# Kernel tuning notes

Measured on AMD Instinct MI355X. Metric: run time of the kernel, lower is better.

The kernel has to match this reference:

```python
import jax, jax.numpy as jnp
import numpy as np

B, C, H, W = 16, 1024, 32, 32  # H*W must equal C (required by matmul(h, fg) in the source)
EPS = 1e-5
NEG_SLOPE = 0.01


def setup_inputs() -> dict:
    key = jax.random.key(0)
    ks = jax.random.split(key, 12)
    s = 1.0 / np.sqrt(C)
    inp = {"x": jax.random.normal(ks[0], (B, C, H, W), jnp.float32)}
    for i, name in enumerate(["f", "g", "h", "c"]):
        inp[f"W{name}"] = jax.random.normal(ks[1 + 2 * i], (C, C), jnp.float32) * s
        inp[f"b{name}"] = jax.random.normal(ks[2 + 2 * i], (C,), jnp.float32) * 0.01
    inp["gamma"] = jnp.ones((C,), jnp.float32)
    inp["beta"] = jnp.zeros((C,), jnp.float32)
    inp["rmean"] = jax.random.normal(ks[9], (C,), jnp.float32) * 0.01
    inp["rvar"] = jax.random.uniform(ks[10], (C,), jnp.float32, 0.5, 1.5)
    return inp


def reference(x, Wf, bf, Wg, bg, Wh, bh, Wc, bc, gamma, beta, rmean, rvar):
    b, c, h_, w_ = x.shape
    n = h_ * w_  # == c by construction
    xf = x.reshape(b, c, n)

    def proj(Wp, bp):  # 1x1 conv == per-pixel channel matmul
        return jnp.einsum('oc,bcn->bon', Wp, xf) + bp[None, :, None]

    f = proj(Wf, bf)              # (B, C, N)
    g = proj(Wg, bg)              # (B, C, N); transposed(1,2) handled in einsum
    hh = proj(Wh, bh)             # (B, C, N)
    scores = jnp.einsum('bcn,bdn->bcd', f, g)        # f @ g^T -> (B, C, C)
    attn = jax.nn.softmax(scores, axis=1)            # softmax over dim=1 (as in source)
    # dropout2d(p=0.5) is identity in eval mode
    hfg = jnp.einsum('bcn,bnd->bcd', hh, attn)       # matmul(h, fg), needs N == C
    hfg = hfg.reshape(b, c, h_, w_)
    y = jnp.einsum('oc,bchw->bohw', Wc, hfg) + bc[None, :, None, None]
    y = jnp.where(y >= 0, y, NEG_SLOPE * y)          # LeakyReLU
    inv = gamma / jnp.sqrt(rvar + EPS)               # BatchNorm (eval mode)
    y = (y - rmean[None, :, None, None]) * inv[None, :, None, None] + beta[None, :, None, None]
    return y + x
```

## Files before the change

kernel.cpp:

```cpp
#include <hip/hip_runtime.h>
#include <cstdint>
#include <cstddef>

using half8  = __attribute__((ext_vector_type(8))) _Float16;
using half4  = __attribute__((ext_vector_type(4))) _Float16;
using float4v = __attribute__((ext_vector_type(4))) float;

#define CD 1024
#define M2 (1024 * 1024)

#define GLD16(gp, lp)                                                          \
    __builtin_amdgcn_global_load_lds(                                          \
        (const __attribute__((address_space(1))) void*)(gp),                   \
        (__attribute__((address_space(3))) void*)(lp), 16, 0, 0)

__global__ void prep_weights(const float* __restrict__ Wf, const float* __restrict__ Wg,
                             const float* __restrict__ Wh, const float* __restrict__ Wc,
                             const float* __restrict__ bf, const float* __restrict__ bg,
                             const float* __restrict__ bh,
                             _Float16* __restrict__ Wfgh, _Float16* __restrict__ WcH,
                             float* __restrict__ bstack) {
    int idx = blockIdx.x * 256 + threadIdx.x;
    if (idx < 3 * M2) {
        const float* s = idx < M2 ? Wf : (idx < 2 * M2 ? Wg : Wh);
        int off = idx & (M2 - 1);
        Wfgh[idx] = (_Float16)s[off];
    } else if (idx < 4 * M2) {
        WcH[idx - 3 * M2] = (_Float16)Wc[idx - 3 * M2];
    } else if (idx < 4 * M2 + 3 * CD) {
        int j = idx - 4 * M2;
        const float* s = j < CD ? bf : (j < 2 * CD ? bg : bh);
        bstack[j] = s[j & (CD - 1)];
    }
}

__global__ void transpose_x(const float* __restrict__ x, _Float16* __restrict__ xT, int b0) {
    __shared__ float tile[32][33];
    int z = blockIdx.z;
    const float* xb = x + (size_t)(b0 + z) * M2;
    _Float16* xTb = xT + (size_t)z * M2;
    int n0 = blockIdx.x * 32, k0 = blockIdx.y * 32;
    int tx = threadIdx.x, ty = threadIdx.y;
#pragma unroll
    for (int i = 0; i < 4; i++)
        tile[ty + i * 8][tx] = xb[(size_t)(k0 + ty + i * 8) * CD + n0 + tx];
    __syncthreads();
#pragma unroll
    for (int i = 0; i < 4; i++)
        xTb[(size_t)(n0 + ty + i * 8) * CD + k0 + tx] = (_Float16)tile[tx][ty + i * 8];
}

__global__ __launch_bounds__(256) void gemv_bch(const float* __restrict__ Wc,
                                                const float* __restrict__ bh,
                                                float* __restrict__ bch) {
    int o = blockIdx.x * 4 + (threadIdx.x >> 6);
    int lane = threadIdx.x & 63;
    float s = 0.f;
    for (int c = lane; c < CD; c += 64) s += Wc[(size_t)o * CD + c] * bh[c];
#pragma unroll
    for (int off = 32; off > 0; off >>= 1) s += __shfl_xor(s, off);
    if (lane == 0) bch[o] = s;
}

__global__ __launch_bounds__(256) void gemm128(const _Float16* __restrict__ A,
                                               const _Float16* __restrict__ B,
                                               _Float16* __restrict__ C) {
    __shared__ __align__(16) _Float16 As[128][32];
    __shared__ __align__(16) _Float16 Bs[128][32];
    int row0 = blockIdx.y * 128, col0 = blockIdx.x * 128;
    int tid = threadIdx.x, lane = tid & 63, wave = tid >> 6;
    int wr = wave >> 1, wc = wave & 1;
    const int srow = lane >> 2;
    const int scol = (lane & 3) * 8;
    const size_t gA0 = (size_t)(row0 + wave * 16 + srow) * 1024 + scol;
    const size_t gA1 = gA0 + (size_t)64 * 1024;
    const size_t gB0 = (size_t)(col0 + wave * 16 + srow) * 1024 + scol;
    const size_t gB1 = gB0 + (size_t)64 * 1024;
    _Float16* ldsA0 = &As[wave * 16][0];
    _Float16* ldsA1 = &As[64 + wave * 16][0];
    _Float16* ldsB0 = &Bs[wave * 16][0];
    _Float16* ldsB1 = &Bs[64 + wave * 16][0];
    float4v acc[4][4] = {};
    const int kq = (lane >> 4) * 8, rl = lane & 15;
    for (int kt = 0; kt < 1024; kt += 32) {
        GLD16(A + gA0 + kt, ldsA0);
        GLD16(A + gA1 + kt, ldsA1);
        GLD16(B + gB0 + kt, ldsB0);
        GLD16(B + gB1 + kt, ldsB1);
        __syncthreads();
        half8 af[4], bfr[4];
#pragma unroll
        for (int m = 0; m < 4; m++) af[m] = *(const half8*)(&As[wr * 64 + m * 16 + rl][kq]);
#pragma unroll
        for (int n = 0; n < 4; n++) bfr[n] = *(const half8*)(&Bs[wc * 64 + n * 16 + rl][kq]);
#pragma unroll
        for (int m = 0; m < 4; m++)
#pragma unroll
            for (int n = 0; n < 4; n++)
                acc[m][n] = __builtin_amdgcn_mfma_f32_16x16x32_f16(af[m], bfr[n], acc[m][n], 0, 0, 0);
        __syncthreads();
    }
#pragma unroll
    for (int m = 0; m < 4; m++)
#pragma unroll
        for (int r = 0; r < 4; r++) {
            int row = row0 + wr * 64 + m * 16 + ((lane >> 4) << 2) + r;
#pragma unroll
            for (int n = 0; n < 4; n++) {
                int col = col0 + wc * 64 + n * 16 + (lane & 15);
                C[(size_t)row * 1024 + col] = (_Float16)acc[m][n][r];
            }
        }
}

__global__ __launch_bounds__(256) void softmax_col(const float* __restrict__ ST,
                                                   _Float16* __restrict__ attnT) {
    int d = blockIdx.x, z = blockIdx.y;
    const float* row = ST + ((size_t)z * CD + d) * CD;
    _Float16* orow = attnT + ((size_t)z * CD + d) * CD;
    int t = threadIdx.x;
    float4v v = *(const float4v*)(row + t * 4);
    float mx = fmaxf(fmaxf(v[0], v[1]), fmaxf(v[2], v[3]));
#pragma unroll
    for (int o = 32; o > 0; o >>= 1) mx = fmaxf(mx, __shfl_xor(mx, o));
    __shared__ float redm[4], reds[4];
    int wave = t >> 6, lane = t & 63;
    if (lane == 0) redm[wave] = mx;
    __syncthreads();
    mx = fmaxf(fmaxf(redm[0], redm[1]), fmaxf(redm[2], redm[3]));
    float e[4];
    float s = 0.f;
#pragma unroll
    for (int i = 0; i < 4; i++) {
        e[i] = __expf(v[i] - mx);
        s += e[i];
    }
#pragma unroll
    for (int o = 32; o > 0; o >>= 1) s += __shfl_xor(s, o);
    if (lane == 0) reds[wave] = s;
    __syncthreads();
    s = reds[0] + reds[1] + reds[2] + reds[3];
    float inv = 1.0f / s;
    half4 ov;
#pragma unroll
    for (int i = 0; i < 4; i++) ov[i] = (_Float16)(e[i] * inv);
    *(half4*)(orow + t * 4) = ov;
}

enum { EP_F16B = 0, EP_F32 = 1, EP_F16 = 2, EP_FIN = 3 };

#define STG_A(T, BUF)                                                          \
    GLD16(gA + (size_t)(T) * 64 + 0 * 8192, &As[BUF][wv * 32 + 0][0]);         \
    GLD16(gA + (size_t)(T) * 64 + 1 * 8192, &As[BUF][wv * 32 + 8][0]);         \
    GLD16(gA + (size_t)(T) * 64 + 2 * 8192, &As[BUF][wv * 32 + 16][0]);        \
    GLD16(gA + (size_t)(T) * 64 + 3 * 8192, &As[BUF][wv * 32 + 24][0]);
#define STG_B(T, BUF)                                                          \
    GLD16(gB + (size_t)(T) * 64 + 0 * 8192, &Bs[BUF][wv * 32 + 0][0]);         \
    GLD16(gB + (size_t)(T) * 64 + 1 * 8192, &Bs[BUF][wv * 32 + 8][0]);         \
    GLD16(gB + (size_t)(T) * 64 + 2 * 8192, &Bs[BUF][wv * 32 + 16][0]);        \
    GLD16(gB + (size_t)(T) * 64 + 3 * 8192, &Bs[BUF][wv * 32 + 24][0]);

#define READS(SET, BUF, COL)                                                   \
    _Pragma("unroll") for (int m = 0; m < 8; m++)                              \
        a##SET[m] = *(const half8*)&As[BUF][wr * 128 + m * 16 + rl][COL];      \
    _Pragma("unroll") for (int n = 0; n < 4; n++)                              \
        b##SET[n] = *(const half8*)&Bs[BUF][wc * 64 + n * 16 + rl][COL];

#define MFMA32(SET)                                                            \
    __builtin_amdgcn_s_setprio(1);                                             \
    _Pragma("unroll") for (int m = 0; m < 8; m++)                              \
        _Pragma("unroll") for (int n = 0; n < 4; n++)                          \
            acc[m][n] = __builtin_amdgcn_mfma_f32_16x16x32_f16(                \
                a##SET[m], b##SET[n], acc[m][n], 0, 0, 0);                     \
    __builtin_amdgcn_s_setprio(0);

#define TILE64(BUF, OBUF, DOSTAGE, STT)                                        \
    {                                                                          \
        asm volatile("s_waitcnt vmcnt(0)" ::: "memory");                       \
        __builtin_amdgcn_sched_barrier(0);                                     \
        __builtin_amdgcn_s_barrier();                                          \
        READS(0, BUF, c0)                                                      \
        if (DOSTAGE) { STG_A(STT, OBUF) }                                      \
        MFMA32(0)                                                              \
        READS(1, BUF, c1)                                                      \
        if (DOSTAGE) { STG_B(STT, OBUF) }                                      \
        MFMA32(1)                                                              \
    }

template <int EPI>
__global__ __launch_bounds__(512, 2) void gemm_nt(
    const _Float16* __restrict__ A, int64_t sA, const _Float16* __restrict__ B, int64_t sB,
    void* __restrict__ Cp, int64_t sC, const float* __restrict__ bias,
    const float* __restrict__ bc, const float* __restrict__ gamma,
    const float* __restrict__ beta, const float* __restrict__ rmean,
    const float* __restrict__ rvar, const float* __restrict__ xres) {
    __shared__ __align__(16) _Float16 As[2][256][64];
    __shared__ __align__(16) _Float16 Bs[2][256][64];
    int z = blockIdx.z;
    const _Float16* Ab = A + (size_t)z * sA;
    const _Float16* Bb = B + (size_t)z * sB;
    int row0 = blockIdx.y * 256, col0 = blockIdx.x * 256;
    int tid = threadIdx.x, lane = tid & 63, wv = tid >> 6;
    int wr = wv >> 2, wc = wv & 3;

    const _Float16* gA = Ab + (size_t)(row0 + wv * 32 + (lane >> 3)) * 1024 +
                         ((lane & 7) ^ (lane >> 3)) * 8;
    const _Float16* gB = Bb + (size_t)(col0 + wv * 32 + (lane >> 3)) * 1024 +
                         ((lane & 7) ^ (lane >> 3)) * 8;

    const int rl = lane & 15;
    const int q = lane >> 4;
    const int c0 = ((q) ^ (rl & 7)) * 8;
    const int c1 = ((q + 4) ^ (rl & 7)) * 8;

    float4v acc[8][4] = {};
    half8 a0[8], b0[4], a1[8], b1[4];

    STG_A(0, 0) STG_B(0, 0)

#pragma unroll 1
    for (int g = 0; g < 7; ++g) {
        int t = 2 * g;
        TILE64(0, 1, 1, t + 1)
        TILE64(1, 0, 1, t + 2)
    }
    TILE64(0, 1, 1, 15)
    TILE64(1, 0, 0, 0)

#pragma unroll
    for (int m = 0; m < 8; m++) {
#pragma unroll
        for (int r = 0; r < 4; r++) {
            int row = row0 + wr * 128 + m * 16 + ((lane >> 4) << 2) + r;
            float add0 = 0.f, mu = 0.f, invs = 1.f, bet = 0.f;
            if constexpr (EPI == EP_F16B) add0 = bias[row];
            if constexpr (EPI == EP_FIN) {
                add0 = bc[row];
                mu = rmean[row];
                invs = gamma[row] * rsqrtf(rvar[row] + 1e-5f);
                bet = beta[row];
            }
#pragma unroll
            for (int n = 0; n < 4; n++) {
                int col = col0 + wc * 64 + n * 16 + (lane & 15);
                float v = acc[m][n][r];
                if constexpr (EPI == EP_F16B) {
                    ((_Float16*)Cp)[(size_t)z * sC + (size_t)row * 1024 + col] = (_Float16)(v + add0);
                } else if constexpr (EPI == EP_F32) {
                    ((float*)Cp)[(size_t)z * sC + (size_t)row * 1024 + col] = v;
                } else if constexpr (EPI == EP_F16) {
                    ((_Float16*)Cp)[(size_t)z * sC + (size_t)row * 1024 + col] = (_Float16)v;
                } else {
                    v += add0;
                    v = v >= 0.f ? v : 0.01f * v;
                    v = (v - mu) * invs + bet;
                    v += xres[(size_t)z * M2 + (size_t)row * 1024 + col];
                    ((float*)Cp)[(size_t)z * sC + (size_t)row * 1024 + col] = v;
                }
            }
        }
    }
}

extern "C" void kernel_launch(void* const* d_in, const int* in_sizes, int n_in,
                              void* d_out, int out_size, void* d_ws, size_t ws_size,
                              hipStream_t stream) {
    const float* x = (const float*)d_in[0];
    const float* Wf = (const float*)d_in[1];
    const float* bf = (const float*)d_in[2];
    const float* Wg = (const float*)d_in[3];
    const float* bg = (const float*)d_in[4];
    const float* Wh = (const float*)d_in[5];
    const float* bh = (const float*)d_in[6];
    const float* Wc = (const float*)d_in[7];
    const float* bc = (const float*)d_in[8];
    const float* gamma = (const float*)d_in[9];
    const float* beta = (const float*)d_in[10];
    const float* rmean = (const float*)d_in[11];
    const float* rvar = (const float*)d_in[12];

    char* p = (char*)d_ws;
    _Float16* Wfgh = (_Float16*)p;
    p += (size_t)3 * M2 * 2;
    _Float16* WcH = (_Float16*)p;
    p += (size_t)M2 * 2;
    float* bstack = (float*)p;
    p += (size_t)3 * CD * 4;
    size_t fixed = (size_t)(p - (char*)d_ws);
    fixed = (fixed + 255) & ~(size_t)255;

    size_t perB = (size_t)2 * M2 + (size_t)6 * M2 + (size_t)4 * M2;
    int nb = 16;
    while (nb > 1 && fixed + (size_t)nb * perB > ws_size) nb >>= 1;

    char* q = (char*)d_ws + fixed;

    {
        int total = 4 * M2 + 3 * CD;
        prep_weights<<<dim3((total + 255) / 256), dim3(256), 0, stream>>>(
            Wf, Wg, Wh, Wc, bf, bg, bh, Wfgh, WcH, bstack);
    }
    {
        _Float16* WhT = (_Float16*)q;
        transpose_x<<<dim3(32, 32, 1), dim3(32, 8), 0, stream>>>(Wh, WhT, 0);
        gemv_bch<<<dim3(256), dim3(256), 0, stream>>>(Wc, bh, bstack + 2 * CD);
        gemm128<<<dim3(8, 8), dim3(256), 0, stream>>>(WcH, WhT, Wfgh + (size_t)2 * M2);
    }

    for (int b0 = 0; b0 < 16; b0 += nb) {
        _Float16* xT = (_Float16*)q;
        _Float16* FGH = (_Float16*)(q + (size_t)nb * 2 * M2);
        float* ST = (float*)(q + (size_t)nb * 8 * M2);
        _Float16* attnT = xT;

        transpose_x<<<dim3(32, 32, nb), dim3(32, 8), 0, stream>>>(x, xT, b0);
        gemm_nt<EP_F16B><<<dim3(4, 12, nb), dim3(512), 0, stream>>>(
            Wfgh, 0, xT, M2, FGH, (int64_t)3 * M2, bstack,
            nullptr, nullptr, nullptr, nullptr, nullptr, nullptr);
        gemm_nt<EP_F32><<<dim3(4, 4, nb), dim3(512), 0, stream>>>(
            FGH + M2, (int64_t)3 * M2, FGH, (int64_t)3 * M2, ST, M2,
            nullptr, nullptr, nullptr, nullptr, nullptr, nullptr, nullptr);
        softmax_col<<<dim3(1024, nb), dim3(256), 0, stream>>>(ST, attnT);
        gemm_nt<EP_FIN><<<dim3(4, 4, nb), dim3(512), 0, stream>>>(
            FGH + (size_t)2 * M2, (int64_t)3 * M2, attnT, M2,
            (float*)d_out + (size_t)b0 * M2, M2,
            nullptr, bc, gamma, beta, rmean, rvar, x + (size_t)b0 * M2);
    }
}
```

Measured before the change: 279.3 us.

## Shrink batched GEMM tiles to 128x128 and split-K the weight-fold GEMM

The main batched GEMM kernel now uses 128x128 tiles with 256 threads instead of 256x256 tiles with 512 threads, which quadruples the grid. This is meant to spread work across more compute units and raise occupancy, since the previous grids were small (e.g. 4x4x16 blocks). The one-off Wc·Wh weight fold GEMM is split four ways along K into fp32 partials, followed by a new reduction kernel, so that it launches more than 64 blocks. In exchange, smaller tiles give less data reuse per block and more global/LDS traffic, and the split-K path adds an extra pass over fp32 partials.

```diff
diff --git a/kernel.cpp b/kernel.cpp
--- a/kernel.cpp
+++ b/kernel.cpp
@@ -62,19 +62,20 @@
     if (lane == 0) bch[o] = s;
 }
 
-__global__ __launch_bounds__(256) void gemm128(const _Float16* __restrict__ A,
-                                               const _Float16* __restrict__ B,
-                                               _Float16* __restrict__ C) {
+__global__ __launch_bounds__(256) void gemm128k(const _Float16* __restrict__ A,
+                                                const _Float16* __restrict__ B,
+                                                float* __restrict__ P) {
     __shared__ __align__(16) _Float16 As[128][32];
     __shared__ __align__(16) _Float16 Bs[128][32];
     int row0 = blockIdx.y * 128, col0 = blockIdx.x * 128;
+    int koff = blockIdx.z * 256;
     int tid = threadIdx.x, lane = tid & 63, wave = tid >> 6;
     int wr = wave >> 1, wc = wave & 1;
     const int srow = lane >> 2;
     const int scol = (lane & 3) * 8;
-    const size_t gA0 = (size_t)(row0 + wave * 16 + srow) * 1024 + scol;
+    const size_t gA0 = (size_t)(row0 + wave * 16 + srow) * 1024 + koff + scol;
     const size_t gA1 = gA0 + (size_t)64 * 1024;
-    const size_t gB0 = (size_t)(col0 + wave * 16 + srow) * 1024 + scol;
+    const size_t gB0 = (size_t)(col0 + wave * 16 + srow) * 1024 + koff + scol;
     const size_t gB1 = gB0 + (size_t)64 * 1024;
     _Float16* ldsA0 = &As[wave * 16][0];
     _Float16* ldsA1 = &As[64 + wave * 16][0];
@@ -82,7 +83,7 @@
     _Float16* ldsB1 = &Bs[64 + wave * 16][0];
     float4v acc[4][4] = {};
     const int kq = (lane >> 4) * 8, rl = lane & 15;
-    for (int kt = 0; kt < 1024; kt += 32) {
+    for (int kt = 0; kt < 256; kt += 32) {
         GLD16(A + gA0 + kt, ldsA0);
         GLD16(A + gA1 + kt, ldsA1);
         GLD16(B + gB0 + kt, ldsB0);
@@ -100,6 +101,7 @@
                 acc[m][n] = __builtin_amdgcn_mfma_f32_16x16x32_f16(af[m], bfr[n], acc[m][n], 0, 0, 0);
         __syncthreads();
     }
+    float* Pz = P + (size_t)blockIdx.z * M2;
 #pragma unroll
     for (int m = 0; m < 4; m++)
 #pragma unroll
@@ -108,9 +110,24 @@
 #pragma unroll
             for (int n = 0; n < 4; n++) {
                 int col = col0 + wc * 64 + n * 16 + (lane & 15);
-                C[(size_t)row * 1024 + col] = (_Float16)acc[m][n][r];
+                Pz[(size_t)row * 1024 + col] = acc[m][n][r];
             }
         }
+}
+
+__global__ __launch_bounds__(256) void reduce_wch(const float* __restrict__ P,
+                                                  _Float16* __restrict__ Wch) {
+    int i = (blockIdx.x * 256 + threadIdx.x) * 4;
+    float4v s = *(const float4v*)(P + i);
+#pragma unroll
+    for (int z = 1; z < 4; z++) {
+        float4v v = *(const float4v*)(P + (size_t)z * M2 + i);
+        s[0] += v[0]; s[1] += v[1]; s[2] += v[2]; s[3] += v[3];
+    }
+    half4 o;
+#pragma unroll
+    for (int j = 0; j < 4; j++) o[j] = (_Float16)s[j];
+    *(half4*)(Wch + i) = o;
 }
 
 __global__ __launch_bounds__(256) void softmax_col(const float* __restrict__ ST,
@@ -161,14 +178,14 @@
     GLD16(gB + (size_t)(T) * 64 + 3 * 8192, &Bs[BUF][wv * 32 + 24][0]);
 
 #define READS(SET, BUF, COL)                                                   \
-    _Pragma("unroll") for (int m = 0; m < 8; m++)                              \
-        a##SET[m] = *(const half8*)&As[BUF][wr * 128 + m * 16 + rl][COL];      \
+    _Pragma("unroll") for (int m = 0; m < 4; m++)                              \
+        a##SET[m] = *(const half8*)&As[BUF][wr * 64 + m * 16 + rl][COL];       \
     _Pragma("unroll") for (int n = 0; n < 4; n++)                              \
         b##SET[n] = *(const half8*)&Bs[BUF][wc * 64 + n * 16 + rl][COL];
 
-#define MFMA32(SET)                                                            \
+#define MFMA16(SET)                                                            \
     __builtin_amdgcn_s_setprio(1);                                             \
-    _Pragma("unroll") for (int m = 0; m < 8; m++)                              \
+    _Pragma("unroll") for (int m = 0; m < 4; m++)                              \
         _Pragma("unroll") for (int n = 0; n < 4; n++)                          \
             acc[m][n] = __builtin_amdgcn_mfma_f32_16x16x32_f16(                \
                 a##SET[m], b##SET[n], acc[m][n], 0, 0, 0);                     \
@@ -181,27 +198,27 @@
         __builtin_amdgcn_s_barrier();                                          \
         READS(0, BUF, c0)                                                      \
         if (DOSTAGE) { STG_A(STT, OBUF) }                                      \
-        MFMA32(0)                                                              \
+        MFMA16(0)                                                              \
         READS(1, BUF, c1)                                                      \
         if (DOSTAGE) { STG_B(STT, OBUF) }                                      \
-        MFMA32(1)                                                              \
+        MFMA16(1)                                                              \
     }
 
 template <int EPI>
-__global__ __launch_bounds__(512, 2) void gemm_nt(
+__global__ __launch_bounds__(256, 2) void gemm_nt(
     const _Float16* __restrict__ A, int64_t sA, const _Float16* __restrict__ B, int64_t sB,
     void* __restrict__ Cp, int64_t sC, const float* __restrict__ bias,
     const float* __restrict__ bc, const float* __restrict__ gamma,
     const float* __restrict__ beta, const float* __restrict__ rmean,
     const float* __restrict__ rvar, const float* __restrict__ xres) {
-    __shared__ __align__(16) _Float16 As[2][256][64];
-    __shared__ __align__(16) _Float16 Bs[2][256][64];
+    __shared__ __align__(16) _Float16 As[2][128][64];
+    __shared__ __align__(16) _Float16 Bs[2][128][64];
     int z = blockIdx.z;
     const _Float16* Ab = A + (size_t)z * sA;
     const _Float16* Bb = B + (size_t)z * sB;
-    int row0 = blockIdx.y * 256, col0 = blockIdx.x * 256;
+    int row0 = blockIdx.y * 128, col0 = blockIdx.x * 128;
     int tid = threadIdx.x, lane = tid & 63, wv = tid >> 6;
-    int wr = wv >> 2, wc = wv & 3;
+    int wr = wv >> 1, wc = wv & 1;
 
     const _Float16* gA = Ab + (size_t)(row0 + wv * 32 + (lane >> 3)) * 1024 +
                          ((lane & 7) ^ (lane >> 3)) * 8;
@@ -213,8 +230,8 @@
     const int c0 = ((q) ^ (rl & 7)) * 8;
     const int c1 = ((q + 4) ^ (rl & 7)) * 8;
 
-    float4v acc[8][4] = {};
-    half8 a0[8], b0[4], a1[8], b1[4];
+    float4v acc[4][4] = {};
+    half8 a0[4], b0[4], a1[4], b1[4];
 
     STG_A(0, 0) STG_B(0, 0)
 
@@ -228,10 +245,10 @@
     TILE64(1, 0, 0, 0)
 
 #pragma unroll
-    for (int m = 0; m < 8; m++) {
+    for (int m = 0; m < 4; m++) {
 #pragma unroll
         for (int r = 0; r < 4; r++) {
-            int row = row0 + wr * 128 + m * 16 + ((lane >> 4) << 2) + r;
+            int row = row0 + wr * 64 + m * 16 + ((lane >> 4) << 2) + r;
             float add0 = 0.f, mu = 0.f, invs = 1.f, bet = 0.f;
             if constexpr (EPI == EP_F16B) add0 = bias[row];
             if constexpr (EPI == EP_FIN) {
@@ -302,9 +319,11 @@
     }
     {
         _Float16* WhT = (_Float16*)q;
+        float* Pk = (float*)(q + (size_t)2 * M2);
         transpose_x<<<dim3(32, 32, 1), dim3(32, 8), 0, stream>>>(Wh, WhT, 0);
         gemv_bch<<<dim3(256), dim3(256), 0, stream>>>(Wc, bh, bstack + 2 * CD);
-        gemm128<<<dim3(8, 8), dim3(256), 0, stream>>>(WcH, WhT, Wfgh + (size_t)2 * M2);
+        gemm128k<<<dim3(8, 8, 4), dim3(256), 0, stream>>>(WcH, WhT, Pk);
+        reduce_wch<<<dim3(M2 / 1024), dim3(256), 0, stream>>>(Pk, Wfgh + (size_t)2 * M2);
     }
 
     for (int b0 = 0; b0 < 16; b0 += nb) {
@@ -314,14 +333,14 @@
         _Float16* attnT = xT;
 
         transpose_x<<<dim3(32, 32, nb), dim3(32, 8), 0, stream>>>(x, xT, b0);
-        gemm_nt<EP_F16B><<<dim3(4, 12, nb), dim3(512), 0, stream>>>(
+        gemm_nt<EP_F16B><<<dim3(8, 24, nb), dim3(256), 0, stream>>>(
             Wfgh, 0, xT, M2, FGH, (int64_t)3 * M2, bstack,
             nullptr, nullptr, nullptr, nullptr, nullptr, nullptr);
-        gemm_nt<EP_F32><<<dim3(4, 4, nb), dim3(512), 0, stream>>>(
+        gemm_nt<EP_F32><<<dim3(8, 8, nb), dim3(256), 0, stream>>>(
             FGH + M2, (int64_t)3 * M2, FGH, (int64_t)3 * M2, ST, M2,
             nullptr, nullptr, nullptr, nullptr, nullptr, nullptr, nullptr);
         softmax_col<<<dim3(1024, nb), dim3(256), 0, stream>>>(ST, attnT);
-        gemm_nt<EP_FIN><<<dim3(4, 4, nb), dim3(512), 0, stream>>>(
+        gemm_nt<EP_FIN><<<dim3(8, 8, nb), dim3(256), 0, stream>>>(
             FGH + (size_t)2 * M2, (int64_t)3 * M2, attnT, M2,
             (float*)d_out + (size_t)b0 * M2, M2,
             nullptr, bc, gamma, beta, rmean, rvar, x + (size_t)b0 * M2);
```

Result: slower. 315.5 us (+13.0%).
